# Performance work log

Measured on AMD Instinct MI355X. Metric: run time of the kernel, lower is better.

## Reference

```python
import jax, jax.numpy as jnp
import numpy as np

SCALE = 4

def setup_inputs() -> dict:
    key = jax.random.key(0)
    # LR image batch in [0,1], as produced by torchvision ToTensor
    x = jax.random.uniform(key, (16, 3, 256, 256), dtype=jnp.float32)
    return {"x": x}

def reference(x) -> jnp.ndarray:
    if SCALE == 1:
        return x
    B, C, H, W = x.shape
    # PIL BICUBIC == Keys cubic kernel with a=-0.5; jax.image 'cubic' uses the
    # same kernel. Upscaling, so no antialias filtering differences apply.
    out_shape = (B, C, H * SCALE, W * SCALE)
    return jax.image.resize(x, out_shape, method="cubic")
```

## Files before the change

### kernel.cpp

```cpp
#include <hip/hip_runtime.h>


#define Hin 256
#define Win 256

#define WK00 -0.0439453125f
#define WK01  0.3896484375f
#define WK02  0.7275390625f
#define WK03 -0.0732421875f
#define WK10 -0.0068359375f
#define WK11  0.0908203125f
#define WK12  0.9638671875f
#define WK13 -0.0478515625f

__global__ __launch_bounds__(256, 4) void cubic_up4(const float* __restrict__ in,
                                                    float* __restrict__ out) {
    const int jx = threadIdx.x;
    const int jy4 = blockIdx.x & 63;
    const int bc = blockIdx.x >> 6;
    const int jy0 = jy4 << 2;

    const float* __restrict__ inp = in + (size_t)bc * (Hin * Win);
    float* __restrict__ outp = out + (size_t)bc * ((size_t)Hin * Win * 16);

    const float WK[4][4] = {{WK00, WK01, WK02, WK03},
                            {WK10, WK11, WK12, WK13},
                            {WK13, WK12, WK11, WK10},
                            {WK03, WK02, WK01, WK00}};

    __shared__ float sv[8][Win + 4];
#pragma unroll
    for (int r = 0; r < 8; ++r) {
        int ry = jy0 - 2 + r;
        ry = ry < 0 ? 0 : (ry > Hin - 1 ? Hin - 1 : ry);
        sv[r][jx + 2] = inp[ry * Win + jx];
    }
    if (jx < 2) {
#pragma unroll
        for (int r = 0; r < 8; ++r) sv[r][jx] = 0.f;
    }
    if (jx >= Win - 2) {
#pragma unroll
        for (int r = 0; r < 8; ++r) sv[r][jx + 4] = 0.f;
    }
    __syncthreads();

    float h[8][4];
    const bool xedge = (jx < 2) | (jx >= Win - 2);
    if (!xedge) {
#pragma unroll
        for (int r = 0; r < 8; ++r) {
            const float* p = &sv[r][jx];
            const float a0 = p[0], a1 = p[1], a2 = p[2], a3 = p[3], a4 = p[4];
            h[r][0] = WK00 * a0 + WK01 * a1 + WK02 * a2 + WK03 * a3;
            h[r][1] = WK10 * a0 + WK11 * a1 + WK12 * a2 + WK13 * a3;
            h[r][2] = WK13 * a1 + WK12 * a2 + WK11 * a3 + WK10 * a4;
            h[r][3] = WK03 * a1 + WK02 * a2 + WK01 * a3 + WK00 * a4;
        }
    } else {
        float wx[4][4];
#pragma unroll
        for (int r = 0; r < 4; ++r) {
            const int o = r >> 1;
            float s = 0.f;
#pragma unroll
            for (int t = 0; t < 4; ++t) {
                const int c = jx - 2 + o + t;
                const float w = (c >= 0 && c < Win) ? WK[r][t] : 0.f;
                wx[r][t] = w;
                s += w;
            }
            const float inv = __builtin_amdgcn_rcpf(s);
#pragma unroll
            for (int t = 0; t < 4; ++t) wx[r][t] *= inv;
        }
#pragma unroll
        for (int r = 0; r < 8; ++r) {
            const float* p = &sv[r][jx];
#pragma unroll
            for (int rx = 0; rx < 4; ++rx) {
                const int o = rx >> 1;
                h[r][rx] = wx[rx][0] * p[o] + wx[rx][1] * p[o + 1] +
                           wx[rx][2] * p[o + 2] + wx[rx][3] * p[o + 3];
            }
        }
    }

    const bool yedge = (jy4 == 0) | (jy4 == 63);
    if (!yedge) {
#pragma unroll
        for (int ty = 0; ty < 4; ++ty) {
#pragma unroll
            for (int ry = 0; ry < 4; ++ry) {
                const int o = ty + (ry >> 1);
                float4 res;
                float* rp = (float*)&res;
#pragma unroll
                for (int rx = 0; rx < 4; ++rx) {
                    rp[rx] = WK[ry][0] * h[o][rx] + WK[ry][1] * h[o + 1][rx] +
                             WK[ry][2] * h[o + 2][rx] + WK[ry][3] * h[o + 3][rx];
                }
                *(float4*)(outp + (size_t)((jy4 << 4) + (ty << 2) + ry) * (Win * 4) +
                           (jx << 2)) = res;
            }
        }
    } else {
#pragma unroll
        for (int ty = 0; ty < 4; ++ty) {
            const int jy = jy0 + ty;
            float wy[4][4];
#pragma unroll
            for (int r = 0; r < 4; ++r) {
                const int o = r >> 1;
                float s = 0.f;
#pragma unroll
                for (int t = 0; t < 4; ++t) {
                    const int c = jy - 2 + o + t;
                    const float w = (c >= 0 && c < Hin) ? WK[r][t] : 0.f;
                    wy[r][t] = w;
                    s += w;
                }
                const float inv = __builtin_amdgcn_rcpf(s);
#pragma unroll
                for (int t = 0; t < 4; ++t) wy[r][t] *= inv;
            }
#pragma unroll
            for (int ry = 0; ry < 4; ++ry) {
                const int o = ty + (ry >> 1);
                float4 res;
                float* rp = (float*)&res;
#pragma unroll
                for (int rx = 0; rx < 4; ++rx) {
                    rp[rx] = wy[ry][0] * h[o][rx] + wy[ry][1] * h[o + 1][rx] +
                             wy[ry][2] * h[o + 2][rx] + wy[ry][3] * h[o + 3][rx];
                }
                *(float4*)(outp + (size_t)((jy4 << 4) + (ty << 2) + ry) * (Win * 4) +
                           (jx << 2)) = res;
            }
        }
    }
}

extern "C" void kernel_launch(void* const* d_in, const int* in_sizes, int n_in,
                              void* d_out, int out_size, void* d_ws, size_t ws_size,
                              hipStream_t stream) {
    const float* x = (const float*)d_in[0];
    float* out = (float*)d_out;
    cubic_up4<<<dim3(48 * 64), dim3(256), 0, stream>>>(x, out);
}
```

Measured before the change: 200.5 us.

## Process three row groups per block with register-prefetched double-buffered LDS

Each block now handles three consecutive 4-row output groups instead of one, giving a grid of 1024 blocks. The next group's eight input rows are prefetched into registers while the current group is computed, and two LDS buffers alternate between groups. The aim is to hide global load latency and amortise block launch and setup. In exchange there are fewer blocks to fill the GPU (1024 over 256 CUs), more register pressure, and the kernel is still bound by the output write bandwidth.

Result: no change. 199.7 us (-0.4%).

```diff
diff --git a/kernel.cpp b/kernel.cpp
--- a/kernel.cpp
+++ b/kernel.cpp
@@ -3,6 +3,8 @@
 
 #define Hin 256
 #define Win 256
+#define GPB 3
+#define LDSW (Win + 4)
 
 #define WK00 -0.0439453125f
 #define WK01  0.3896484375f
@@ -16,126 +18,160 @@
 __global__ __launch_bounds__(256, 4) void cubic_up4(const float* __restrict__ in,
                                                     float* __restrict__ out) {
     const int jx = threadIdx.x;
-    const int jy4 = blockIdx.x & 63;
-    const int bc = blockIdx.x >> 6;
-    const int jy0 = jy4 << 2;
 
-    const float* __restrict__ inp = in + (size_t)bc * (Hin * Win);
-    float* __restrict__ outp = out + (size_t)bc * ((size_t)Hin * Win * 16);
+    __shared__ float sv[2][8][LDSW];
+
+    if (jx < 2) {
+#pragma unroll
+        for (int b = 0; b < 2; ++b)
+#pragma unroll
+            for (int r = 0; r < 8; ++r) sv[b][r][jx] = 0.f;
+    }
+    if (jx >= Win - 2) {
+#pragma unroll
+        for (int b = 0; b < 2; ++b)
+#pragma unroll
+            for (int r = 0; r < 8; ++r) sv[b][r][jx + 4] = 0.f;
+    }
 
     const float WK[4][4] = {{WK00, WK01, WK02, WK03},
                             {WK10, WK11, WK12, WK13},
                             {WK13, WK12, WK11, WK10},
                             {WK03, WK02, WK01, WK00}};
 
-    __shared__ float sv[8][Win + 4];
-#pragma unroll
-    for (int r = 0; r < 8; ++r) {
-        int ry = jy0 - 2 + r;
-        ry = ry < 0 ? 0 : (ry > Hin - 1 ? Hin - 1 : ry);
-        sv[r][jx + 2] = inp[ry * Win + jx];
-    }
-    if (jx < 2) {
-#pragma unroll
-        for (int r = 0; r < 8; ++r) sv[r][jx] = 0.f;
-    }
-    if (jx >= Win - 2) {
-#pragma unroll
-        for (int r = 0; r < 8; ++r) sv[r][jx + 4] = 0.f;
-    }
-    __syncthreads();
+    const int g0 = blockIdx.x * GPB;
 
-    float h[8][4];
-    const bool xedge = (jx < 2) | (jx >= Win - 2);
-    if (!xedge) {
+    float pre[8];
+    {
+        const int bc = g0 >> 6;
+        const int jy0 = (g0 & 63) << 2;
+        const float* __restrict__ inp = in + (size_t)bc * (Hin * Win);
 #pragma unroll
         for (int r = 0; r < 8; ++r) {
-            const float* p = &sv[r][jx];
-            const float a0 = p[0], a1 = p[1], a2 = p[2], a3 = p[3], a4 = p[4];
-            h[r][0] = WK00 * a0 + WK01 * a1 + WK02 * a2 + WK03 * a3;
-            h[r][1] = WK10 * a0 + WK11 * a1 + WK12 * a2 + WK13 * a3;
-            h[r][2] = WK13 * a1 + WK12 * a2 + WK11 * a3 + WK10 * a4;
-            h[r][3] = WK03 * a1 + WK02 * a2 + WK01 * a3 + WK00 * a4;
-        }
-    } else {
-        float wx[4][4];
-#pragma unroll
-        for (int r = 0; r < 4; ++r) {
-            const int o = r >> 1;
-            float s = 0.f;
-#pragma unroll
-            for (int t = 0; t < 4; ++t) {
-                const int c = jx - 2 + o + t;
-                const float w = (c >= 0 && c < Win) ? WK[r][t] : 0.f;
-                wx[r][t] = w;
-                s += w;
-            }
-            const float inv = __builtin_amdgcn_rcpf(s);
-#pragma unroll
-            for (int t = 0; t < 4; ++t) wx[r][t] *= inv;
-        }
-#pragma unroll
-        for (int r = 0; r < 8; ++r) {
-            const float* p = &sv[r][jx];
-#pragma unroll
-            for (int rx = 0; rx < 4; ++rx) {
-                const int o = rx >> 1;
-                h[r][rx] = wx[rx][0] * p[o] + wx[rx][1] * p[o + 1] +
-                           wx[rx][2] * p[o + 2] + wx[rx][3] * p[o + 3];
-            }
+            int ry = jy0 - 2 + r;
+            ry = ry < 0 ? 0 : (ry > Hin - 1 ? Hin - 1 : ry);
+            pre[r] = inp[ry * Win + jx];
         }
     }
 
-    const bool yedge = (jy4 == 0) | (jy4 == 63);
-    if (!yedge) {
 #pragma unroll
-        for (int ty = 0; ty < 4; ++ty) {
+    for (int i = 0; i < GPB; ++i) {
+        const int g = g0 + i;
+        const int jy4 = g & 63;
+        const int jy0 = jy4 << 2;
+        float* __restrict__ outp = out + (size_t)(g >> 6) * ((size_t)Hin * Win * 16);
+
+        float(*sb)[LDSW] = sv[i & 1];
+
 #pragma unroll
-            for (int ry = 0; ry < 4; ++ry) {
-                const int o = ty + (ry >> 1);
-                float4 res;
-                float* rp = (float*)&res;
+        for (int r = 0; r < 8; ++r) sb[r][jx + 2] = pre[r];
+        __syncthreads();
+
+        if (i + 1 < GPB) {
+            const int gn = g + 1;
+            const int bcn = gn >> 6;
+            const int jy0n = (gn & 63) << 2;
+            const float* __restrict__ inpn = in + (size_t)bcn * (Hin * Win);
 #pragma unroll
-                for (int rx = 0; rx < 4; ++rx) {
-                    rp[rx] = WK[ry][0] * h[o][rx] + WK[ry][1] * h[o + 1][rx] +
-                             WK[ry][2] * h[o + 2][rx] + WK[ry][3] * h[o + 3][rx];
-                }
-                *(float4*)(outp + (size_t)((jy4 << 4) + (ty << 2) + ry) * (Win * 4) +
-                           (jx << 2)) = res;
+            for (int r = 0; r < 8; ++r) {
+                int ry = jy0n - 2 + r;
+                ry = ry < 0 ? 0 : (ry > Hin - 1 ? Hin - 1 : ry);
+                pre[r] = inpn[ry * Win + jx];
             }
         }
-    } else {
+
+        float h[8][4];
+        const bool xedge = (jx < 2) | (jx >= Win - 2);
+        if (!xedge) {
 #pragma unroll
-        for (int ty = 0; ty < 4; ++ty) {
-            const int jy = jy0 + ty;
-            float wy[4][4];
+            for (int r = 0; r < 8; ++r) {
+                const float* p = &sb[r][jx];
+                const float a0 = p[0], a1 = p[1], a2 = p[2], a3 = p[3], a4 = p[4];
+                h[r][0] = WK00 * a0 + WK01 * a1 + WK02 * a2 + WK03 * a3;
+                h[r][1] = WK10 * a0 + WK11 * a1 + WK12 * a2 + WK13 * a3;
+                h[r][2] = WK13 * a1 + WK12 * a2 + WK11 * a3 + WK10 * a4;
+                h[r][3] = WK03 * a1 + WK02 * a2 + WK01 * a3 + WK00 * a4;
+            }
+        } else {
+            float wx[4][4];
 #pragma unroll
             for (int r = 0; r < 4; ++r) {
                 const int o = r >> 1;
                 float s = 0.f;
 #pragma unroll
                 for (int t = 0; t < 4; ++t) {
-                    const int c = jy - 2 + o + t;
-                    const float w = (c >= 0 && c < Hin) ? WK[r][t] : 0.f;
-                    wy[r][t] = w;
+                    const int c = jx - 2 + o + t;
+                    const float w = (c >= 0 && c < Win) ? WK[r][t] : 0.f;
+                    wx[r][t] = w;
                     s += w;
                 }
                 const float inv = __builtin_amdgcn_rcpf(s);
 #pragma unroll
-                for (int t = 0; t < 4; ++t) wy[r][t] *= inv;
+                for (int t = 0; t < 4; ++t) wx[r][t] *= inv;
             }
 #pragma unroll
-            for (int ry = 0; ry < 4; ++ry) {
-                const int o = ty + (ry >> 1);
-                float4 res;
-                float* rp = (float*)&res;
+            for (int r = 0; r < 8; ++r) {
+                const float* p = &sb[r][jx];
 #pragma unroll
                 for (int rx = 0; rx < 4; ++rx) {
-                    rp[rx] = wy[ry][0] * h[o][rx] + wy[ry][1] * h[o + 1][rx] +
-                             wy[ry][2] * h[o + 2][rx] + wy[ry][3] * h[o + 3][rx];
+                    const int o = rx >> 1;
+                    h[r][rx] = wx[rx][0] * p[o] + wx[rx][1] * p[o + 1] +
+                               wx[rx][2] * p[o + 2] + wx[rx][3] * p[o + 3];
                 }
-                *(float4*)(outp + (size_t)((jy4 << 4) + (ty << 2) + ry) * (Win * 4) +
-                           (jx << 2)) = res;
+            }
+        }
+
+        const bool yedge = (jy4 == 0) | (jy4 == 63);
+        if (!yedge) {
+#pragma unroll
+            for (int ty = 0; ty < 4; ++ty) {
+#pragma unroll
+                for (int ry = 0; ry < 4; ++ry) {
+                    const int o = ty + (ry >> 1);
+                    float4 res;
+                    float* rp = (float*)&res;
+#pragma unroll
+                    for (int rx = 0; rx < 4; ++rx) {
+                        rp[rx] = WK[ry][0] * h[o][rx] + WK[ry][1] * h[o + 1][rx] +
+                                 WK[ry][2] * h[o + 2][rx] + WK[ry][3] * h[o + 3][rx];
+                    }
+                    *(float4*)(outp + (size_t)((jy4 << 4) + (ty << 2) + ry) * (Win * 4) +
+                               (jx << 2)) = res;
+                }
+            }
+        } else {
+#pragma unroll
+            for (int ty = 0; ty < 4; ++ty) {
+                const int jy = jy0 + ty;
+                float wy[4][4];
+#pragma unroll
+                for (int r = 0; r < 4; ++r) {
+                    const int o = r >> 1;
+                    float s = 0.f;
+#pragma unroll
+                    for (int t = 0; t < 4; ++t) {
+                        const int c = jy - 2 + o + t;
+                        const float w = (c >= 0 && c < Hin) ? WK[r][t] : 0.f;
+                        wy[r][t] = w;
+                        s += w;
+                    }
+                    const float inv = __builtin_amdgcn_rcpf(s);
+#pragma unroll
+                    for (int t = 0; t < 4; ++t) wy[r][t] *= inv;
+                }
+#pragma unroll
+                for (int ry = 0; ry < 4; ++ry) {
+                    const int o = ty + (ry >> 1);
+                    float4 res;
+                    float* rp = (float*)&res;
+#pragma unroll
+                    for (int rx = 0; rx < 4; ++rx) {
+                        rp[rx] = wy[ry][0] * h[o][rx] + wy[ry][1] * h[o + 1][rx] +
+                                 wy[ry][2] * h[o + 2][rx] + wy[ry][3] * h[o + 3][rx];
+                    }
+                    *(float4*)(outp + (size_t)((jy4 << 4) + (ty << 2) + ry) * (Win * 4) +
+                               (jx << 2)) = res;
+                }
             }
         }
     }
@@ -146,5 +182,5 @@
                               hipStream_t stream) {
     const float* x = (const float*)d_in[0];
     float* out = (float*)d_out;
-    cubic_up4<<<dim3(48 * 64), dim3(256), 0, stream>>>(x, out);
+    cubic_up4<<<dim3(1024), dim3(256), 0, stream>>>(x, out);
 }
```
